# Kernel optimization log

Hardware: AMD Instinct MI355X
Metric: run time of the kernel (lower is better)

Reference implementation:

```python
import jax, jax.numpy as jnp
import numpy as np


def setup_inputs() -> dict:
    key = jax.random.key(0)
    k1, k2 = jax.random.split(key)
    # x: (b, t, C, H, W) feature maps
    x = jax.random.normal(k1, (2, 32, 128, 64, 64), dtype=jnp.float32)
    # attn_mask: (n_heads, b, t, t, h, w) attention weights at coarse resolution
    attn_mask = jax.random.uniform(k2, (4, 2, 32, 32, 16, 16), dtype=jnp.float32)
    return {"x": x, "attn_mask": attn_mask}


def reference(x, attn_mask):
    # TemporalAggregationMode.ATT_GROUP, pad_mask=None branch.
    g, b, t, _, h, w = attn_mask.shape
    B, T, C, H, W = x.shape
    c = C // g  # channels per head-group

    attn = attn_mask.reshape(g * b * t, t, h, w)
    if H > w:
        # bilinear upsample, half-pixel centers == torch align_corners=False
        attn = jax.image.resize(attn, (g * b * t, t, H, W), method='bilinear')
    else:
        k = w // H  # AvgPool2d(kernel_size=k), stride=k
        attn = attn.reshape(g * b * t, t, H, k, W, k).mean(axis=(3, 5))
    attn = attn.reshape(g, b, t, t, H, W)

    # x.chunk(n_heads, dim=2): contiguous channel groups -> (b, t, g, c, H, W)
    xg = x.reshape(b, t, g, c, H, W)

    # out[g,b,q,c,h,w] = sum_k attn[g,b,q,k,h,w] * xg[b,k,g,c,h,w]
    # fused per-pixel temporal contraction (no (g,b,t,t,c,H,W) blowup)
    out = jnp.einsum('gbqkhw,bkgchw->bqgchw', attn, xg)

    # torch.cat over groups along channel dim == reshape groups back into C
    return out.reshape(b, t, C, H, W)
```

## Files before the change

kernel.cpp:

```cpp
#include <hip/hip_runtime.h>

typedef float f4 __attribute__((ext_vector_type(4)));

#define Gn 4
#define Bn 2
#define Tn 32
#define Cn 128
#define CG 32
#define Hn 64
#define Wn 64
#define HC 16
#define WC 16

__global__ __launch_bounds__(256, 3)
void temporal_agg_kernel(const float* __restrict__ x,
                         const float* __restrict__ attn,
                         float* __restrict__ out) {
    const int bid   = blockIdx.x;
    const int whalf = bid & 1;
    const int h     = (bid >> 1) & 63;
    const int b     = (bid >> 7) & 1;
    const int g     = bid >> 8;

    const int tid = threadIdx.x;

    const float chf = 0.25f * (float)h - 0.375f;
    const float h0f = floorf(chf);
    const float fh  = chf - h0f;
    int h0 = (int)h0f;
    int h1 = h0 + 1;
    h0 = min(max(h0, 0), HC - 1);
    h1 = min(max(h1, 0), HC - 1);

    __shared__ float Ah[Tn][10][36];

    const int wcb = whalf * 8 - 1;
    const float* abase = attn + (size_t)(g * Bn + b) * (Tn * Tn * HC * WC);
    #pragma unroll 8
    for (int i = 0; i < 64; ++i) {
        int idx = tid + 256 * i;
        int wc = idx & 15;
        int k  = (idx >> 4) & 31;
        int q  = idx >> 9;
        const float* p = abase + (size_t)(q * Tn + k) * (HC * WC);
        float v0 = p[h0 * WC + wc];
        float v1 = p[h1 * WC + wc];
        float ah = v0 + fh * (v1 - v0);
        int j = wc - wcb;
        if (j >= 0 && j < 10) Ah[k][j][q] = ah;
        if (whalf == 0 && wc == 0)  Ah[k][0][q] = ah;
        if (whalf == 1 && wc == 15) Ah[k][9][q] = ah;
    }
    __syncthreads();

    const int qslot = tid & 7;
    const int wl    = (tid >> 3) & 7;
    const int cslot = tid >> 6;
    const int q0    = qslot * 4;
    const int wfine = whalf * 32 + wl * 4;
    const int off_hw = h * Wn + wfine;

    for (int chalf = 0; chalf < 2; ++chalf) {
        f4 acc[4][4];
        #pragma unroll
        for (int qq = 0; qq < 4; ++qq)
            #pragma unroll
            for (int cc = 0; cc < 4; ++cc)
                acc[qq][cc] = (f4)0.0f;

        const int cbase = g * CG + chalf * 16 + cslot * 4;
        const float* xb = x + (size_t)b * (Tn * Cn * Hn * Wn)
                            + (size_t)cbase * (Hn * Wn) + off_hw;

        #pragma unroll 2
        for (int k = 0; k < Tn; ++k) {
            f4 t0 = *(const f4*)&Ah[k][wl    ][q0];
            f4 t1 = *(const f4*)&Ah[k][wl + 1][q0];
            f4 t2 = *(const f4*)&Ah[k][wl + 2][q0];

            f4 xv[4];
            const float* xk = xb + (size_t)k * (Cn * Hn * Wn);
            #pragma unroll
            for (int cc = 0; cc < 4; ++cc)
                xv[cc] = *(const f4*)(xk + cc * (Hn * Wn));

            #pragma unroll
            for (int qq = 0; qq < 4; ++qq) {
                f4 a;
                a.x = 0.375f * t0[qq] + 0.625f * t1[qq];
                a.y = 0.125f * t0[qq] + 0.875f * t1[qq];
                a.z = 0.875f * t1[qq] + 0.125f * t2[qq];
                a.w = 0.625f * t1[qq] + 0.375f * t2[qq];
                #pragma unroll
                for (int cc = 0; cc < 4; ++cc)
                    acc[qq][cc] += a * xv[cc];
            }
        }

        #pragma unroll
        for (int qq = 0; qq < 4; ++qq) {
            const int q = q0 + qq;
            float* ob = out + ((size_t)(b * Tn + q) * Cn + cbase) * (Hn * Wn) + off_hw;
            #pragma unroll
            for (int cc = 0; cc < 4; ++cc)
                *(f4*)(ob + cc * (Hn * Wn)) = acc[qq][cc];
        }
    }
}

extern "C" void kernel_launch(void* const* d_in, const int* in_sizes, int n_in,
                              void* d_out, int out_size, void* d_ws, size_t ws_size,
                              hipStream_t stream) {
    const float* x    = (const float*)d_in[0];
    const float* attn = (const float*)d_in[1];
    float* out        = (float*)d_out;
    temporal_agg_kernel<<<dim3(Gn * Bn * Hn * 2), dim3(256), 0, stream>>>(x, attn, out);
}
```

Before: 329.6 us.

## Split query range across blocks, vectorize attn loads, prefetch x across k

Each block now handles half the query rows (16) and all 32 group channels in one pass, doubling the grid to 2048 blocks and shrinking the shared attention tile. The attention staging loop uses float4 loads with fewer iterations. The temporal loop register-prefetches the next k's x values so loads overlap compute, and launch bounds ask for 4 blocks per SM. The trade-off is that x is read twice as often across blocks (once per q-half) and register pressure rises from the prefetch buffer.

```diff
diff --git a/kernel.cpp b/kernel.cpp
--- a/kernel.cpp
+++ b/kernel.cpp
@@ -6,23 +6,23 @@
 #define Bn 2
 #define Tn 32
 #define Cn 128
-#define CG 32
 #define Hn 64
 #define Wn 64
 #define HC 16
 #define WC 16
+#define HW (Hn * Wn)
 
-__global__ __launch_bounds__(256, 3)
+__global__ __launch_bounds__(256, 4)
 void temporal_agg_kernel(const float* __restrict__ x,
                          const float* __restrict__ attn,
                          float* __restrict__ out) {
     const int bid   = blockIdx.x;
-    const int whalf = bid & 1;
-    const int h     = (bid >> 1) & 63;
-    const int b     = (bid >> 7) & 1;
-    const int g     = bid >> 8;
-
-    const int tid = threadIdx.x;
+    const int qhalf = bid & 1;
+    const int whalf = (bid >> 1) & 1;
+    const int h     = (bid >> 2) & 63;
+    const int b     = (bid >> 8) & 1;
+    const int g     = bid >> 9;
+    const int tid   = threadIdx.x;
 
     const float chf = 0.25f * (float)h - 0.375f;
     const float h0f = floorf(chf);
@@ -32,79 +32,97 @@
     h0 = min(max(h0, 0), HC - 1);
     h1 = min(max(h1, 0), HC - 1);
 
-    __shared__ float Ah[Tn][10][36];
+    __shared__ float Ah[Tn][10][20];
 
     const int wcb = whalf * 8 - 1;
+    const int qb  = qhalf * 16;
     const float* abase = attn + (size_t)(g * Bn + b) * (Tn * Tn * HC * WC);
-    #pragma unroll 8
-    for (int i = 0; i < 64; ++i) {
+
+    #pragma unroll
+    for (int i = 0; i < 8; ++i) {
         int idx = tid + 256 * i;
-        int wc = idx & 15;
-        int k  = (idx >> 4) & 31;
-        int q  = idx >> 9;
-        const float* p = abase + (size_t)(q * Tn + k) * (HC * WC);
-        float v0 = p[h0 * WC + wc];
-        float v1 = p[h1 * WC + wc];
-        float ah = v0 + fh * (v1 - v0);
-        int j = wc - wcb;
-        if (j >= 0 && j < 10) Ah[k][j][q] = ah;
-        if (whalf == 0 && wc == 0)  Ah[k][0][q] = ah;
-        if (whalf == 1 && wc == 15) Ah[k][9][q] = ah;
+        int c4 = idx & 3;
+        int k  = (idx >> 2) & 31;
+        int ql = idx >> 7;
+        const float* p = abase + (size_t)((qb + ql) * Tn + k) * (HC * WC);
+        f4 v0 = *(const f4*)(p + h0 * WC + 4 * c4);
+        f4 v1 = *(const f4*)(p + h1 * WC + 4 * c4);
+        f4 ah = v0 + fh * (v1 - v0);
+        #pragma unroll
+        for (int e = 0; e < 4; ++e) {
+            int wc = 4 * c4 + e;
+            int j = wc - wcb;
+            if (j >= 0 && j < 10) Ah[k][j][ql] = ah[e];
+            if (whalf == 0 && wc == 0)  Ah[k][0][ql] = ah[e];
+            if (whalf == 1 && wc == 15) Ah[k][9][ql] = ah[e];
+        }
     }
     __syncthreads();
 
-    const int qslot = tid & 7;
-    const int wl    = (tid >> 3) & 7;
-    const int cslot = tid >> 6;
-    const int q0    = qslot * 4;
+    const int qslot = tid & 3;
+    const int wl    = (tid >> 2) & 7;
+    const int cslot = tid >> 5;
+    const int ql0   = qslot * 4;
     const int wfine = whalf * 32 + wl * 4;
     const int off_hw = h * Wn + wfine;
+    const int cbase  = g * 32 + cslot * 4;
 
-    for (int chalf = 0; chalf < 2; ++chalf) {
-        f4 acc[4][4];
+    const float* xb = x + (size_t)b * (Tn * Cn * HW)
+                        + (size_t)cbase * HW + off_hw;
+    const size_t kstride = (size_t)Cn * HW;
+
+    f4 acc[4][4];
+    #pragma unroll
+    for (int qq = 0; qq < 4; ++qq)
         #pragma unroll
-        for (int qq = 0; qq < 4; ++qq)
-            #pragma unroll
-            for (int cc = 0; cc < 4; ++cc)
-                acc[qq][cc] = (f4)0.0f;
+        for (int cc = 0; cc < 4; ++cc)
+            acc[qq][cc] = (f4)0.0f;
 
-        const int cbase = g * CG + chalf * 16 + cslot * 4;
-        const float* xb = x + (size_t)b * (Tn * Cn * Hn * Wn)
-                            + (size_t)cbase * (Hn * Wn) + off_hw;
+    f4 xv[4];
+    #pragma unroll
+    for (int cc = 0; cc < 4; ++cc)
+        xv[cc] = *(const f4*)(xb + cc * HW);
 
-        #pragma unroll 2
-        for (int k = 0; k < Tn; ++k) {
-            f4 t0 = *(const f4*)&Ah[k][wl    ][q0];
-            f4 t1 = *(const f4*)&Ah[k][wl + 1][q0];
-            f4 t2 = *(const f4*)&Ah[k][wl + 2][q0];
+#define COMPUTE(kk)                                                     \
+    do {                                                                \
+        f4 t0 = *(const f4*)&Ah[kk][wl    ][ql0];                       \
+        f4 t1 = *(const f4*)&Ah[kk][wl + 1][ql0];                       \
+        f4 t2 = *(const f4*)&Ah[kk][wl + 2][ql0];                       \
+        _Pragma("unroll")                                               \
+        for (int qq = 0; qq < 4; ++qq) {                                \
+            f4 a;                                                       \
+            a.x = 0.375f * t0[qq] + 0.625f * t1[qq];                    \
+            a.y = 0.125f * t0[qq] + 0.875f * t1[qq];                    \
+            a.z = 0.875f * t1[qq] + 0.125f * t2[qq];                    \
+            a.w = 0.625f * t1[qq] + 0.375f * t2[qq];                    \
+            _Pragma("unroll")                                           \
+            for (int cc = 0; cc < 4; ++cc)                              \
+                acc[qq][cc] += a * xv[cc];                              \
+        }                                                               \
+    } while (0)
 
-            f4 xv[4];
-            const float* xk = xb + (size_t)k * (Cn * Hn * Wn);
-            #pragma unroll
-            for (int cc = 0; cc < 4; ++cc)
-                xv[cc] = *(const f4*)(xk + cc * (Hn * Wn));
+    #pragma unroll 4
+    for (int k = 0; k < Tn - 1; ++k) {
+        const float* xn_p = xb + (size_t)(k + 1) * kstride;
+        f4 xn[4];
+        #pragma unroll
+        for (int cc = 0; cc < 4; ++cc)
+            xn[cc] = *(const f4*)(xn_p + cc * HW);
+        COMPUTE(k);
+        #pragma unroll
+        for (int cc = 0; cc < 4; ++cc)
+            xv[cc] = xn[cc];
+    }
+    COMPUTE(Tn - 1);
+#undef COMPUTE
 
-            #pragma unroll
-            for (int qq = 0; qq < 4; ++qq) {
-                f4 a;
-                a.x = 0.375f * t0[qq] + 0.625f * t1[qq];
-                a.y = 0.125f * t0[qq] + 0.875f * t1[qq];
-                a.z = 0.875f * t1[qq] + 0.125f * t2[qq];
-                a.w = 0.625f * t1[qq] + 0.375f * t2[qq];
-                #pragma unroll
-                for (int cc = 0; cc < 4; ++cc)
-                    acc[qq][cc] += a * xv[cc];
-            }
-        }
-
+    #pragma unroll
+    for (int qq = 0; qq < 4; ++qq) {
+        const int q = qb + ql0 + qq;
+        float* ob = out + ((size_t)(b * Tn + q) * Cn + cbase) * HW + off_hw;
         #pragma unroll
-        for (int qq = 0; qq < 4; ++qq) {
-            const int q = q0 + qq;
-            float* ob = out + ((size_t)(b * Tn + q) * Cn + cbase) * (Hn * Wn) + off_hw;
-            #pragma unroll
-            for (int cc = 0; cc < 4; ++cc)
-                *(f4*)(ob + cc * (Hn * Wn)) = acc[qq][cc];
-        }
+        for (int cc = 0; cc < 4; ++cc)
+            *(f4*)(ob + cc * HW) = acc[qq][cc];
     }
 }
 
@@ -114,5 +132,5 @@
     const float* x    = (const float*)d_in[0];
     const float* attn = (const float*)d_in[1];
     float* out        = (float*)d_out;
-    temporal_agg_kernel<<<dim3(Gn * Bn * Hn * 2), dim3(256), 0, stream>>>(x, attn, out);
+    temporal_agg_kernel<<<dim3(Gn * Bn * Hn * 2 * 2), dim3(256), 0, stream>>>(x, attn, out);
 }
```

Measured after the change: 484.8 us. 47.1% more time.

## Split channel halves across blocks and software-pipeline x loads with staged attention

Applied to the files above, without the earlier changes.

The kernel now launches twice as many blocks of 512 threads, with each block handling one channel half instead of looping over both. The horizontally interpolated attention is staged in shared memory as two 16-timestep halves and loaded with vector reads. x loads are issued two steps ahead through a triple register buffer. Output uses nontemporal stores. The aim is more parallelism and latency hiding for the memory-bound x stream, at the cost of recomputing the attention staging in every block and adding extra barriers.

```diff
diff --git a/kernel.cpp b/kernel.cpp
--- a/kernel.cpp
+++ b/kernel.cpp
@@ -6,23 +6,23 @@
 #define Bn 2
 #define Tn 32
 #define Cn 128
-#define CG 32
 #define Hn 64
 #define Wn 64
 #define HC 16
 #define WC 16
+#define HW (Hn * Wn)
 
-__global__ __launch_bounds__(256, 3)
+__global__ __launch_bounds__(512, 2)
 void temporal_agg_kernel(const float* __restrict__ x,
                          const float* __restrict__ attn,
                          float* __restrict__ out) {
     const int bid   = blockIdx.x;
-    const int whalf = bid & 1;
-    const int h     = (bid >> 1) & 63;
-    const int b     = (bid >> 7) & 1;
-    const int g     = bid >> 8;
-
-    const int tid = threadIdx.x;
+    const int chalf = bid & 1;
+    const int whalf = (bid >> 1) & 1;
+    const int h     = (bid >> 2) & 63;
+    const int b     = (bid >> 8) & 1;
+    const int g     = bid >> 9;
+    const int tid   = threadIdx.x;
 
     const float chf = 0.25f * (float)h - 0.375f;
     const float h0f = floorf(chf);
@@ -32,80 +32,109 @@
     h0 = min(max(h0, 0), HC - 1);
     h1 = min(max(h1, 0), HC - 1);
 
-    __shared__ float Ah[Tn][10][36];
+    __shared__ float Ah[16][10][36];
 
     const int wcb = whalf * 8 - 1;
     const float* abase = attn + (size_t)(g * Bn + b) * (Tn * Tn * HC * WC);
-    #pragma unroll 8
-    for (int i = 0; i < 64; ++i) {
-        int idx = tid + 256 * i;
-        int wc = idx & 15;
-        int k  = (idx >> 4) & 31;
-        int q  = idx >> 9;
-        const float* p = abase + (size_t)(q * Tn + k) * (HC * WC);
-        float v0 = p[h0 * WC + wc];
-        float v1 = p[h1 * WC + wc];
-        float ah = v0 + fh * (v1 - v0);
-        int j = wc - wcb;
-        if (j >= 0 && j < 10) Ah[k][j][q] = ah;
-        if (whalf == 0 && wc == 0)  Ah[k][0][q] = ah;
-        if (whalf == 1 && wc == 15) Ah[k][9][q] = ah;
-    }
-    __syncthreads();
 
-    const int qslot = tid & 7;
+#define PHASE1(kb)                                                          \
+    do {                                                                    \
+        _Pragma("unroll")                                                   \
+        for (int i = 0; i < 4; ++i) {                                       \
+            int idx = tid + 512 * i;                         \
+            int c4 = idx & 3;                                               \
+            int kl = (idx >> 2) & 15;                                       \
+            int q  = idx >> 6;                                              \
+            const float* p = abase + (size_t)(q * Tn + (kb) + kl) * (HC * WC); \
+            f4 v0 = *(const f4*)(p + h0 * WC + 4 * c4);                     \
+            f4 v1 = *(const f4*)(p + h1 * WC + 4 * c4);                     \
+            f4 ah = v0 + fh * (v1 - v0);                                    \
+            _Pragma("unroll")                                               \
+            for (int e = 0; e < 4; ++e) {                                   \
+                int wc = 4 * c4 + e;                                        \
+                int j = wc - wcb;                                           \
+                if (j >= 0 && j < 10) Ah[kl][j][q] = ah[e];                 \
+                if (whalf == 0 && wc == 0)  Ah[kl][0][q] = ah[e];           \
+                if (whalf == 1 && wc == 15) Ah[kl][9][q] = ah[e];           \
+            }                                                               \
+        }                                                                   \
+    } while (0)
+
+    const int cslot = tid & 7;
     const int wl    = (tid >> 3) & 7;
-    const int cslot = tid >> 6;
+    const int qslot = tid >> 6;
     const int q0    = qslot * 4;
     const int wfine = whalf * 32 + wl * 4;
     const int off_hw = h * Wn + wfine;
+    const int cbase  = g * 32 + chalf * 16 + cslot * 2;
 
-    for (int chalf = 0; chalf < 2; ++chalf) {
-        f4 acc[4][4];
-        #pragma unroll
-        for (int qq = 0; qq < 4; ++qq)
-            #pragma unroll
-            for (int cc = 0; cc < 4; ++cc)
-                acc[qq][cc] = (f4)0.0f;
+    const float* xb = x + (size_t)b * (Tn * Cn * HW) + (size_t)cbase * HW + off_hw;
+    const size_t kstride = (size_t)Cn * HW;
 
-        const int cbase = g * CG + chalf * 16 + cslot * 4;
-        const float* xb = x + (size_t)b * (Tn * Cn * Hn * Wn)
-                            + (size_t)cbase * (Hn * Wn) + off_hw;
+    f4 acc[4][2];
+    #pragma unroll
+    for (int qq = 0; qq < 4; ++qq) {
+        acc[qq][0] = (f4)0.0f;
+        acc[qq][1] = (f4)0.0f;
+    }
 
-        #pragma unroll 2
-        for (int k = 0; k < Tn; ++k) {
-            f4 t0 = *(const f4*)&Ah[k][wl    ][q0];
-            f4 t1 = *(const f4*)&Ah[k][wl + 1][q0];
-            f4 t2 = *(const f4*)&Ah[k][wl + 2][q0];
+#define LOADX(dst, kk)                                                      \
+    do {                                                                    \
+        const float* xk = xb + (size_t)(kk) * kstride;                      \
+        (dst)[0] = *(const f4*)(xk);                                        \
+        (dst)[1] = *(const f4*)(xk + HW);                                   \
+    } while (0)
 
-            f4 xv[4];
-            const float* xk = xb + (size_t)k * (Cn * Hn * Wn);
-            #pragma unroll
-            for (int cc = 0; cc < 4; ++cc)
-                xv[cc] = *(const f4*)(xk + cc * (Hn * Wn));
+#define COMPUTE(kk, bb)                                                     \
+    do {                                                                    \
+        f4 t0 = *(const f4*)&Ah[(kk) & 15][wl    ][q0];                     \
+        f4 t1 = *(const f4*)&Ah[(kk) & 15][wl + 1][q0];                     \
+        f4 t2 = *(const f4*)&Ah[(kk) & 15][wl + 2][q0];                     \
+        _Pragma("unroll")                                                   \
+        for (int qq = 0; qq < 4; ++qq) {                                    \
+            f4 a;                                                           \
+            a.x = 0.375f * t0[qq] + 0.625f * t1[qq];                        \
+            a.y = 0.125f * t0[qq] + 0.875f * t1[qq];                        \
+            a.z = 0.875f * t1[qq] + 0.125f * t2[qq];                        \
+            a.w = 0.625f * t1[qq] + 0.375f * t2[qq];                        \
+            acc[qq][0] += a * (bb)[0];                                      \
+            acc[qq][1] += a * (bb)[1];                                      \
+        }                                                                   \
+    } while (0)
 
-            #pragma unroll
-            for (int qq = 0; qq < 4; ++qq) {
-                f4 a;
-                a.x = 0.375f * t0[qq] + 0.625f * t1[qq];
-                a.y = 0.125f * t0[qq] + 0.875f * t1[qq];
-                a.z = 0.875f * t1[qq] + 0.125f * t2[qq];
-                a.w = 0.625f * t1[qq] + 0.375f * t2[qq];
-                #pragma unroll
-                for (int cc = 0; cc < 4; ++cc)
-                    acc[qq][cc] += a * xv[cc];
-            }
-        }
+    f4 buf[3][2];
+    LOADX(buf[0], 0);
+    LOADX(buf[1], 1);
 
-        #pragma unroll
-        for (int qq = 0; qq < 4; ++qq) {
-            const int q = q0 + qq;
-            float* ob = out + ((size_t)(b * Tn + q) * Cn + cbase) * (Hn * Wn) + off_hw;
-            #pragma unroll
-            for (int cc = 0; cc < 4; ++cc)
-                *(f4*)(ob + cc * (Hn * Wn)) = acc[qq][cc];
-        }
+    PHASE1(0);
+    __syncthreads();
+
+    #pragma unroll
+    for (int k = 0; k < 16; ++k) {
+        LOADX(buf[(k + 2) % 3], k + 2);
+        COMPUTE(k, buf[k % 3]);
     }
+
+    __syncthreads();
+    PHASE1(16);
+    __syncthreads();
+
+    #pragma unroll
+    for (int k = 16; k < 32; ++k) {
+        if (k < 30) LOADX(buf[(k + 2) % 3], k + 2);
+        COMPUTE(k, buf[k % 3]);
+    }
+
+    #pragma unroll
+    for (int qq = 0; qq < 4; ++qq) {
+        const int q = q0 + qq;
+        float* ob = out + ((size_t)(b * Tn + q) * Cn + cbase) * HW + off_hw;
+        __builtin_nontemporal_store(acc[qq][0], (f4*)ob);
+        __builtin_nontemporal_store(acc[qq][1], (f4*)(ob + HW));
+    }
+#undef PHASE1
+#undef LOADX
+#undef COMPUTE
 }
 
 extern "C" void kernel_launch(void* const* d_in, const int* in_sizes, int n_in,
@@ -114,5 +143,5 @@
     const float* x    = (const float*)d_in[0];
     const float* attn = (const float*)d_in[1];
     float* out        = (float*)d_out;
-    temporal_agg_kernel<<<dim3(Gn * Bn * Hn * 2), dim3(256), 0, stream>>>(x, attn, out);
+    temporal_agg_kernel<<<dim3(Gn * Bn * Hn * 2 * 2), dim3(512), 0, stream>>>(x, attn, out);
 }
```

Result: slower. 1.044 ms (+216.6%).
